# Performance work log

Measured on AMD Instinct MI355X. Metric: run time of the kernel, lower is better.

Reference implementation:

```python
import jax, jax.numpy as jnp
import numpy as np

N_NODES = 100000
N_EDGES = 1600000
D_IN = 64
D_OUT = 64


def setup_inputs() -> dict:
    key = jax.random.key(0)
    k1, k2, k3, k4, k5 = jax.random.split(key, 5)
    features = jax.random.normal(k1, (N_NODES, D_IN), dtype=jnp.float32)
    edge_rows = jax.random.randint(k2, (N_EDGES,), 0, N_NODES, dtype=jnp.int32)
    edge_cols = jax.random.randint(k3, (N_EDGES,), 0, N_NODES, dtype=jnp.int32)
    edge_vals = jax.random.uniform(k4, (N_EDGES,), dtype=jnp.float32)
    # glorot_uniform init for the dense projection weight
    limit = np.sqrt(6.0 / (D_IN + D_OUT)).astype(np.float32)
    weight = jax.random.uniform(k5, (D_IN, D_OUT), dtype=jnp.float32,
                                minval=-limit, maxval=limit)
    return {"features": features, "edge_rows": edge_rows,
            "edge_cols": edge_cols, "edge_vals": edge_vals, "weight": weight}


def reference(features, edge_rows, edge_cols, edge_vals, weight):
    # SpMM: (adj @ features) via edge-list gather + segment_sum
    gathered = features[edge_cols] * edge_vals[:, None]        # [E, D_IN]
    agg = jax.ops.segment_sum(gathered, edge_rows,
                              num_segments=N_NODES)            # [N, D_IN]
    # Dense projection + ReLU
    return jax.nn.relu(agg @ weight)                           # [N, D_OUT]
```

## Files before the change

### kernel.cpp

```cpp
#include <hip/hip_runtime.h>

#define D 64
#define OVF_CAP 262144


template <int SLOTS>
__global__ void scatter_slot_kernel(const int* __restrict__ erows,
                                    const int* __restrict__ ecols,
                                    const float* __restrict__ evals,
                                    int* __restrict__ cnt,
                                    int2* __restrict__ pairs,
                                    int4* __restrict__ ovf,
                                    int* __restrict__ ovfCnt,
                                    int n_edges, int rows_per_slice) {
    const int slice = blockIdx.x & 7;
    const int rlo   = slice * rows_per_slice;
    const int rhi   = rlo + rows_per_slice;
    const int sub   = blockIdx.x >> 3;
    const int t     = sub * blockDim.x + threadIdx.x;
    const int strid = (gridDim.x >> 3) * blockDim.x;

    for (int e = t; e < n_edges; e += strid) {
        int   r = erows[e];
        int   c = ecols[e];
        float v = evals[e];
        if (r >= rlo && r < rhi) {
            int pos = atomicAdd(&cnt[r], 1);
            if (pos < SLOTS) {
                pairs[(size_t)r * SLOTS + pos] = make_int2(c, __float_as_int(v));
            } else {
                int oi = atomicAdd(ovfCnt, 1);
                if (oi < OVF_CAP)
                    ovf[oi] = make_int4(r, c, __float_as_int(v), 0);
            }
        }
    }
}

template <int SLOTS>
__global__ void __launch_bounds__(256)
fused_slot_kernel(const float* __restrict__ feat, const int* __restrict__ cnt,
                  const int2* __restrict__ pairs, const float* __restrict__ W,
                  const int* __restrict__ ovfCnt, float* __restrict__ out,
                  int n_rows) {
    __shared__ float sW[D * D];
    __shared__ float srow[4][D];

    for (int i = threadIdx.x; i < D * D; i += 256)
        sW[i] = W[i];

    const int  w      = threadIdx.x >> 6;
    const int  lane   = threadIdx.x & 63;
    const int  row    = blockIdx.x * 4 + w;
    const bool doRelu = (*ovfCnt == 0);

    float acc = 0.0f;
    if (row < n_rows) {
        int m = min(cnt[row], SLOTS);
        int px = 0, py = 0;
        if (lane < SLOTS) {
            int2 p = pairs[(size_t)row * SLOTS + lane];
            px = p.x; py = p.y;
        }
        int k = 0;
        for (; k + 4 <= m; k += 4) {
            int c0 = __shfl(px, k + 0), b0 = __shfl(py, k + 0);
            int c1 = __shfl(px, k + 1), b1 = __shfl(py, k + 1);
            int c2 = __shfl(px, k + 2), b2 = __shfl(py, k + 2);
            int c3 = __shfl(px, k + 3), b3 = __shfl(py, k + 3);
            float f0 = feat[(size_t)c0 * D + lane];
            float f1 = feat[(size_t)c1 * D + lane];
            float f2 = feat[(size_t)c2 * D + lane];
            float f3 = feat[(size_t)c3 * D + lane];
            acc = fmaf(f0, __int_as_float(b0), acc);
            acc = fmaf(f1, __int_as_float(b1), acc);
            acc = fmaf(f2, __int_as_float(b2), acc);
            acc = fmaf(f3, __int_as_float(b3), acc);
        }
        for (; k < m; ++k) {
            int c = __shfl(px, k), b = __shfl(py, k);
            acc = fmaf(feat[(size_t)c * D + lane], __int_as_float(b), acc);
        }
    }
    srow[w][lane] = acc;
    __syncthreads();

    float o = 0.0f;
#pragma unroll
    for (int kk = 0; kk < D; ++kk)
        o = fmaf(srow[w][kk], sW[kk * D + lane], o);

    if (row < n_rows)
        out[(size_t)row * D + lane] = doRelu ? fmaxf(o, 0.0f) : o;
}

__global__ void __launch_bounds__(256)
ovf_kernel(const float* __restrict__ feat, const float* __restrict__ W,
           const int4* __restrict__ ovf, const int* __restrict__ ovfCnt,
           float* __restrict__ out) {
    int n = *ovfCnt;
    if (n > OVF_CAP) n = OVF_CAP;
    if (n == 0) return;
    const int lane = threadIdx.x & 63;
    const int wave = (blockIdx.x * blockDim.x + threadIdx.x) >> 6;
    const int nw   = (gridDim.x * blockDim.x) >> 6;
    for (int i = wave; i < n; i += nw) {
        int4  e = ovf[i];
        float v = __int_as_float(e.z);
        float f = feat[(size_t)e.y * D + lane];
        float acc = 0.0f;
#pragma unroll
        for (int k = 0; k < D; ++k)
            acc = fmaf(__shfl(f, k), W[k * D + lane], acc);
        unsafeAtomicAdd(&out[(size_t)e.x * D + lane], v * acc);
    }
}

__global__ void relu_fix_kernel(float* __restrict__ out,
                                const int* __restrict__ ovfCnt, int n_elems) {
    if (*ovfCnt == 0) return;
    int i = blockIdx.x * blockDim.x + threadIdx.x;
    int stride = gridDim.x * blockDim.x;
    for (; i < n_elems; i += stride)
        out[i] = fmaxf(out[i], 0.0f);
}

__global__ void hist_kernel(const int* __restrict__ erows, int* __restrict__ cur,
                            int n_edges) {
    int i = blockIdx.x * blockDim.x + threadIdx.x;
    int stride = gridDim.x * blockDim.x;
    for (int e = i; e < n_edges; e += stride)
        atomicAdd(&cur[erows[e]], 1);
}

__global__ void __launch_bounds__(256)
scan_block_reduce(const int* __restrict__ cnt, int* __restrict__ bs, int n) {
    __shared__ int s[256];
    int i = blockIdx.x * 256 + threadIdx.x;
    s[threadIdx.x] = (i < n) ? cnt[i] : 0;
    __syncthreads();
    for (int off = 128; off > 0; off >>= 1) {
        if (threadIdx.x < (unsigned)off) s[threadIdx.x] += s[threadIdx.x + off];
        __syncthreads();
    }
    if (threadIdx.x == 0) bs[blockIdx.x] = s[0];
}

__global__ void __launch_bounds__(1024)
scan_top(int* __restrict__ bs, int nblk, int* __restrict__ rowStartN) {
    __shared__ int s[1024];
    int t = threadIdx.x;
    int x = (t < nblk) ? bs[t] : 0;
    s[t] = x;
    __syncthreads();
    for (int off = 1; off < 1024; off <<= 1) {
        int y = (t >= off) ? s[t - off] : 0;
        __syncthreads();
        s[t] += y;
        __syncthreads();
    }
    if (t < nblk) bs[t] = s[t] - x;
    if (t == 1023) *rowStartN = s[1023];
}

__global__ void __launch_bounds__(256)
scan_final(int* __restrict__ cur, const int* __restrict__ bs,
           int* __restrict__ rowStart, int n) {
    __shared__ int s[256];
    int t = threadIdx.x;
    int i = blockIdx.x * 256 + t;
    int x = (i < n) ? cur[i] : 0;
    s[t] = x;
    __syncthreads();
    for (int off = 1; off < 256; off <<= 1) {
        int y = (t >= off) ? s[t - off] : 0;
        __syncthreads();
        s[t] += y;
        __syncthreads();
    }
    int excl = s[t] - x + bs[blockIdx.x];
    if (i < n) { rowStart[i] = excl; cur[i] = excl; }
}

__global__ void scatter_kernel(const int* __restrict__ erows,
                               const int* __restrict__ ecols,
                               const float* __restrict__ evals,
                               int* __restrict__ cur, int2* __restrict__ pairs,
                               int n_edges) {
    int i = blockIdx.x * blockDim.x + threadIdx.x;
    int stride = gridDim.x * blockDim.x;
    for (int e = i; e < n_edges; e += stride) {
        int pos = atomicAdd(&cur[erows[e]], 1);
        pairs[pos] = make_int2(ecols[e], __float_as_int(evals[e]));
    }
}

__global__ void __launch_bounds__(256)
fused_kernel(const float* __restrict__ feat, const int* __restrict__ rowStart,
             const int2* __restrict__ pairs, const float* __restrict__ W,
             float* __restrict__ out, int n_rows) {
    __shared__ float sW[D * D];
    __shared__ float srow[4][D];
    for (int i = threadIdx.x; i < D * D; i += 256) sW[i] = W[i];
    const int w = threadIdx.x >> 6, lane = threadIdx.x & 63;
    const int row = blockIdx.x * 4 + w;
    float acc = 0.0f;
    if (row < n_rows) {
        int s = rowStart[row], e = rowStart[row + 1], i = s;
        for (; i + 4 <= e; i += 4) {
            int2 p0 = pairs[i + 0], p1 = pairs[i + 1];
            int2 p2 = pairs[i + 2], p3 = pairs[i + 3];
            float f0 = feat[(size_t)p0.x * D + lane];
            float f1 = feat[(size_t)p1.x * D + lane];
            float f2 = feat[(size_t)p2.x * D + lane];
            float f3 = feat[(size_t)p3.x * D + lane];
            acc = fmaf(f0, __int_as_float(p0.y), acc);
            acc = fmaf(f1, __int_as_float(p1.y), acc);
            acc = fmaf(f2, __int_as_float(p2.y), acc);
            acc = fmaf(f3, __int_as_float(p3.y), acc);
        }
        for (; i < e; ++i) {
            int2 p = pairs[i];
            acc = fmaf(feat[(size_t)p.x * D + lane], __int_as_float(p.y), acc);
        }
    }
    srow[w][lane] = acc;
    __syncthreads();
    float o = 0.0f;
#pragma unroll
    for (int k = 0; k < D; ++k) o = fmaf(srow[w][k], sW[k * D + lane], o);
    if (row < n_rows) out[(size_t)row * D + lane] = fmaxf(o, 0.0f);
}

__global__ void agg_kernel(const float* __restrict__ feat,
                           const int* __restrict__ erows,
                           const int* __restrict__ ecols,
                           const float* __restrict__ evals,
                           float* __restrict__ agg, int n_edges) {
    int gid = blockIdx.x * blockDim.x + threadIdx.x;
    int group = gid >> 4, lane4 = gid & 15;
    int stride = (gridDim.x * blockDim.x) >> 4;
    for (int e = group; e < n_edges; e += stride) {
        int r = erows[e], c = ecols[e];
        float v = evals[e];
        const float4 f = *reinterpret_cast<const float4*>(feat + (size_t)c * D + lane4 * 4);
        float* dst = agg + (size_t)r * D + lane4 * 4;
        unsafeAtomicAdd(dst + 0, f.x * v);
        unsafeAtomicAdd(dst + 1, f.y * v);
        unsafeAtomicAdd(dst + 2, f.z * v);
        unsafeAtomicAdd(dst + 3, f.w * v);
    }
}

__global__ void __launch_bounds__(256)
proj_kernel(const float* __restrict__ agg, const float* __restrict__ W,
            float* __restrict__ out, int n_rows) {
    __shared__ float sW[D * D];
    __shared__ float srow[4][D];
    for (int i = threadIdx.x; i < D * D; i += 256) sW[i] = W[i];
    __syncthreads();
    const int rg = threadIdx.x >> 6, j = threadIdx.x & 63;
    for (int row0 = blockIdx.x * 4; row0 < n_rows; row0 += gridDim.x * 4) {
        int r = row0 + rg;
        float v = (r < n_rows) ? agg[(size_t)r * D + j] : 0.0f;
        srow[rg][j] = v;
        __syncthreads();
        float acc = 0.0f;
#pragma unroll
        for (int k = 0; k < D; ++k) acc = fmaf(srow[rg][k], sW[k * D + j], acc);
        if (r < n_rows) out[(size_t)r * D + j] = fmaxf(acc, 0.0f);
        __syncthreads();
    }
}

extern "C" void kernel_launch(void* const* d_in, const int* in_sizes, int n_in,
                              void* d_out, int out_size, void* d_ws, size_t ws_size,
                              hipStream_t stream) {
    const float* feat  = (const float*)d_in[0];
    const int*   erows = (const int*)  d_in[1];
    const int*   ecols = (const int*)  d_in[2];
    const float* evals = (const float*)d_in[3];
    const float* W     = (const float*)d_in[4];
    float*       out   = (float*)d_out;

    const int n_edges = in_sizes[1];
    const int n_nodes = in_sizes[0] / D;

    auto align256 = [](size_t x) { return (x + 255) & ~(size_t)255; };

    size_t off_cnt    = 0;
    size_t off_ovfCnt = align256((size_t)n_nodes * 4);
    size_t off_ovf    = align256(off_ovfCnt + 4);
    size_t off_pairs  = align256(off_ovf + (size_t)OVF_CAP * 16);
    size_t need64     = off_pairs + (size_t)n_nodes * 64 * 8;
    size_t need32     = off_pairs + (size_t)n_nodes * 32 * 8;

    const int rows_per_slice = (n_nodes + 7) / 8;

    if (ws_size >= need64 || ws_size >= need32) {
        char* ws     = (char*)d_ws;
        int*  cnt    = (int*) (ws + off_cnt);
        int*  ovfCnt = (int*) (ws + off_ovfCnt);
        int4* ovf    = (int4*)(ws + off_ovf);
        int2* pairs  = (int2*)(ws + off_pairs);

        hipMemsetAsync(cnt, 0, (size_t)n_nodes * 4, stream);
        hipMemsetAsync(ovfCnt, 0, 4, stream);

        if (ws_size >= need64) {
            scatter_slot_kernel<64><<<2048, 256, 0, stream>>>(
                erows, ecols, evals, cnt, pairs, ovf, ovfCnt, n_edges, rows_per_slice);
            fused_slot_kernel<64><<<(n_nodes + 3) / 4, 256, 0, stream>>>(
                feat, cnt, pairs, W, ovfCnt, out, n_nodes);
        } else {
            scatter_slot_kernel<32><<<2048, 256, 0, stream>>>(
                erows, ecols, evals, cnt, pairs, ovf, ovfCnt, n_edges, rows_per_slice);
            fused_slot_kernel<32><<<(n_nodes + 3) / 4, 256, 0, stream>>>(
                feat, cnt, pairs, W, ovfCnt, out, n_nodes);
        }
        ovf_kernel<<<256, 256, 0, stream>>>(feat, W, ovf, ovfCnt, out);
        relu_fix_kernel<<<1024, 256, 0, stream>>>(out, ovfCnt, n_nodes * D);
        return;
    }

    const int nblk = (n_nodes + 255) / 256;
    size_t off_rowStart = 0;
    size_t off_cur      = align256(off_rowStart + (size_t)(n_nodes + 1) * 4);
    size_t off_bs       = align256(off_cur + (size_t)n_nodes * 4);
    size_t off_p        = align256(off_bs + (size_t)nblk * 4);
    size_t ws_needed    = off_p + (size_t)n_edges * 8;

    if (ws_size >= ws_needed && nblk <= 1024) {
        char* ws = (char*)d_ws;
        int*  rowStart = (int*) (ws + off_rowStart);
        int*  cur      = (int*) (ws + off_cur);
        int*  bs       = (int*) (ws + off_bs);
        int2* pairs    = (int2*)(ws + off_p);

        hipMemsetAsync(cur, 0, (size_t)n_nodes * 4, stream);
        hist_kernel<<<2048, 256, 0, stream>>>(erows, cur, n_edges);
        scan_block_reduce<<<nblk, 256, 0, stream>>>(cur, bs, n_nodes);
        scan_top<<<1, 1024, 0, stream>>>(bs, nblk, rowStart + n_nodes);
        scan_final<<<nblk, 256, 0, stream>>>(cur, bs, rowStart, n_nodes);
        scatter_kernel<<<2048, 256, 0, stream>>>(erows, ecols, evals, cur, pairs, n_edges);
        fused_kernel<<<(n_nodes + 3) / 4, 256, 0, stream>>>(feat, rowStart, pairs, W, out, n_nodes);
    } else {
        hipMemsetAsync(out, 0, (size_t)n_nodes * D * 4, stream);
        agg_kernel<<<2048, 256, 0, stream>>>(feat, erows, ecols, evals, out, n_edges);
        proj_kernel<<<2048, 256, 0, stream>>>(out, W, out, n_nodes);
    }
}
```

Measured before the change: 267.6 us.

## Gather bf16 features, unroll edge scatter, use persistent rows and shuffle projection

Features are converted to a bf16 copy in the workspace so that the random-row gather in the fused SpMM kernel moves half the bytes. The scatter kernel now uses 4 row slices instead of 8 and handles four edges per iteration. The fused kernel becomes a grid-stride persistent loop over rows, reads only the valid pairs, and does the 64x64 projection with lane shuffles instead of a shared-memory row buffer and barrier. Rounding features to bf16 loses precision relative to the fp32 reference, and the extra conversion pass adds its own read and write of the feature matrix.

```diff
diff --git a/kernel.cpp b/kernel.cpp
--- a/kernel.cpp
+++ b/kernel.cpp
@@ -1,10 +1,31 @@
 #include <hip/hip_runtime.h>
 
 #define D 64
-#define OVF_CAP 262144
-
-
-template <int SLOTS>
+#define OVF_CAP 65536
+
+
+__device__ inline unsigned short f32_to_bf16_rne(float x) {
+    unsigned u = __float_as_uint(x);
+    unsigned r = (u + 0x7FFFu + ((u >> 16) & 1u)) >> 16;
+    return (unsigned short)r;
+}
+
+__global__ void f2bf_kernel(const float4* __restrict__ in,
+                            ushort4* __restrict__ out, int n4) {
+    int i = blockIdx.x * blockDim.x + threadIdx.x;
+    int stride = gridDim.x * blockDim.x;
+    for (; i < n4; i += stride) {
+        float4 f = in[i];
+        ushort4 u;
+        u.x = f32_to_bf16_rne(f.x);
+        u.y = f32_to_bf16_rne(f.y);
+        u.z = f32_to_bf16_rne(f.z);
+        u.w = f32_to_bf16_rne(f.w);
+        out[i] = u;
+    }
+}
+
+template <int SLOTS, int NSLICE>
 __global__ void scatter_slot_kernel(const int* __restrict__ erows,
                                     const int* __restrict__ ecols,
                                     const float* __restrict__ evals,
@@ -13,55 +34,112 @@
                                     int4* __restrict__ ovf,
                                     int* __restrict__ ovfCnt,
                                     int n_edges, int rows_per_slice) {
-    const int slice = blockIdx.x & 7;
+    const int slice = blockIdx.x & (NSLICE - 1);
     const int rlo   = slice * rows_per_slice;
     const int rhi   = rlo + rows_per_slice;
-    const int sub   = blockIdx.x >> 3;
+    const int sub   = blockIdx.x / NSLICE;
     const int t     = sub * blockDim.x + threadIdx.x;
-    const int strid = (gridDim.x >> 3) * blockDim.x;
-
-    for (int e = t; e < n_edges; e += strid) {
-        int   r = erows[e];
-        int   c = ecols[e];
-        float v = evals[e];
+    const int strid = (gridDim.x / NSLICE) * blockDim.x;
+
+    auto handle = [&](int r, int c, float v) {
         if (r >= rlo && r < rhi) {
             int pos = atomicAdd(&cnt[r], 1);
             if (pos < SLOTS) {
                 pairs[(size_t)r * SLOTS + pos] = make_int2(c, __float_as_int(v));
             } else {
                 int oi = atomicAdd(ovfCnt, 1);
-                if (oi < OVF_CAP)
-                    ovf[oi] = make_int4(r, c, __float_as_int(v), 0);
+                if (oi < OVF_CAP) ovf[oi] = make_int4(r, c, __float_as_int(v), 0);
             }
         }
-    }
+    };
+
+    int e = t;
+    for (; e + 3 * strid < n_edges; e += 4 * strid) {
+        int e0 = e, e1 = e + strid, e2 = e + 2 * strid, e3 = e + 3 * strid;
+        int   r0 = erows[e0], r1 = erows[e1], r2 = erows[e2], r3 = erows[e3];
+        int   c0 = ecols[e0], c1 = ecols[e1], c2 = ecols[e2], c3 = ecols[e3];
+        float v0 = evals[e0], v1 = evals[e1], v2 = evals[e2], v3 = evals[e3];
+        handle(r0, c0, v0);
+        handle(r1, c1, v1);
+        handle(r2, c2, v2);
+        handle(r3, c3, v3);
+    }
+    for (; e < n_edges; e += strid)
+        handle(erows[e], ecols[e], evals[e]);
 }
 
 template <int SLOTS>
 __global__ void __launch_bounds__(256)
-fused_slot_kernel(const float* __restrict__ feat, const int* __restrict__ cnt,
-                  const int2* __restrict__ pairs, const float* __restrict__ W,
-                  const int* __restrict__ ovfCnt, float* __restrict__ out,
-                  int n_rows) {
+fused_slot_bf16(const unsigned short* __restrict__ fb,
+                const int* __restrict__ cnt, const int2* __restrict__ pairs,
+                const float* __restrict__ W, const int* __restrict__ ovfCnt,
+                float* __restrict__ out, int n_rows) {
     __shared__ float sW[D * D];
-    __shared__ float srow[4][D];
-
-    for (int i = threadIdx.x; i < D * D; i += 256)
-        sW[i] = W[i];
+    for (int i = threadIdx.x; i < D * D; i += 256) sW[i] = W[i];
+    __syncthreads();
 
     const int  w      = threadIdx.x >> 6;
     const int  lane   = threadIdx.x & 63;
-    const int  row    = blockIdx.x * 4 + w;
     const bool doRelu = (*ovfCnt == 0);
 
-    float acc = 0.0f;
-    if (row < n_rows) {
+    for (int row = blockIdx.x * 4 + w; row < n_rows; row += gridDim.x * 4) {
         int m = min(cnt[row], SLOTS);
         int px = 0, py = 0;
-        if (lane < SLOTS) {
+        if (lane < m) {
             int2 p = pairs[(size_t)row * SLOTS + lane];
             px = p.x; py = p.y;
         }
+        float acc = 0.0f;
+        int k = 0;
+        for (; k + 4 <= m; k += 4) {
+            int c0 = __shfl(px, k + 0), b0 = __shfl(py, k + 0);
+            int c1 = __shfl(px, k + 1), b1 = __shfl(py, k + 1);
+            int c2 = __shfl(px, k + 2), b2 = __shfl(py, k + 2);
+            int c3 = __shfl(px, k + 3), b3 = __shfl(py, k + 3);
+            float f0 = __uint_as_float((unsigned)fb[(size_t)c0 * D + lane] << 16);
+            float f1 = __uint_as_float((unsigned)fb[(size_t)c1 * D + lane] << 16);
+            float f2 = __uint_as_float((unsigned)fb[(size_t)c2 * D + lane] << 16);
+            float f3 = __uint_as_float((unsigned)fb[(size_t)c3 * D + lane] << 16);
+            acc = fmaf(f0, __int_as_float(b0), acc);
+            acc = fmaf(f1, __int_as_float(b1), acc);
+            acc = fmaf(f2, __int_as_float(b2), acc);
+            acc = fmaf(f3, __int_as_float(b3), acc);
+        }
+        for (; k < m; ++k) {
+            int c = __shfl(px, k), b = __shfl(py, k);
+            acc = fmaf(__uint_as_float((unsigned)fb[(size_t)c * D + lane] << 16),
+                       __int_as_float(b), acc);
+        }
+
+        float o = 0.0f;
+#pragma unroll
+        for (int kk = 0; kk < D; ++kk)
+            o = fmaf(__shfl(acc, kk), sW[kk * D + lane], o);
+
+        out[(size_t)row * D + lane] = doRelu ? fmaxf(o, 0.0f) : o;
+    }
+}
+
+template <int SLOTS>
+__global__ void __launch_bounds__(256)
+fused_slot_f32(const float* __restrict__ feat, const int* __restrict__ cnt,
+               const int2* __restrict__ pairs, const float* __restrict__ W,
+               const int* __restrict__ ovfCnt, float* __restrict__ out,
+               int n_rows) {
+    __shared__ float sW[D * D];
+    for (int i = threadIdx.x; i < D * D; i += 256) sW[i] = W[i];
+    __syncthreads();
+    const int  w      = threadIdx.x >> 6;
+    const int  lane   = threadIdx.x & 63;
+    const bool doRelu = (*ovfCnt == 0);
+    for (int row = blockIdx.x * 4 + w; row < n_rows; row += gridDim.x * 4) {
+        int m = min(cnt[row], SLOTS);
+        int px = 0, py = 0;
+        if (lane < m) {
+            int2 p = pairs[(size_t)row * SLOTS + lane];
+            px = p.x; py = p.y;
+        }
+        float acc = 0.0f;
         int k = 0;
         for (; k + 4 <= m; k += 4) {
             int c0 = __shfl(px, k + 0), b0 = __shfl(py, k + 0);
@@ -81,17 +159,12 @@
             int c = __shfl(px, k), b = __shfl(py, k);
             acc = fmaf(feat[(size_t)c * D + lane], __int_as_float(b), acc);
         }
-    }
-    srow[w][lane] = acc;
-    __syncthreads();
-
-    float o = 0.0f;
+        float o = 0.0f;
 #pragma unroll
-    for (int kk = 0; kk < D; ++kk)
-        o = fmaf(srow[w][kk], sW[kk * D + lane], o);
-
-    if (row < n_rows)
+        for (int kk = 0; kk < D; ++kk)
+            o = fmaf(__shfl(acc, kk), sW[kk * D + lane], o);
         out[(size_t)row * D + lane] = doRelu ? fmaxf(o, 0.0f) : o;
+    }
 }
 
 __global__ void __launch_bounds__(256)
@@ -129,8 +202,7 @@
                             int n_edges) {
     int i = blockIdx.x * blockDim.x + threadIdx.x;
     int stride = gridDim.x * blockDim.x;
-    for (int e = i; e < n_edges; e += stride)
-        atomicAdd(&cur[erows[e]], 1);
+    for (int e = i; e < n_edges; e += stride) atomicAdd(&cur[erows[e]], 1);
 }
 
 __global__ void __launch_bounds__(256)
@@ -291,35 +363,41 @@
     size_t off_cnt    = 0;
     size_t off_ovfCnt = align256((size_t)n_nodes * 4);
     size_t off_ovf    = align256(off_ovfCnt + 4);
-    size_t off_pairs  = align256(off_ovf + (size_t)OVF_CAP * 16);
-    size_t need64     = off_pairs + (size_t)n_nodes * 64 * 8;
-    size_t need32     = off_pairs + (size_t)n_nodes * 32 * 8;
-
-    const int rows_per_slice = (n_nodes + 7) / 8;
-
-    if (ws_size >= need64 || ws_size >= need32) {
+    size_t off_fb     = align256(off_ovf + (size_t)OVF_CAP * 16);
+    size_t off_pairs  = align256(off_fb + (size_t)n_nodes * D * 2);
+    size_t need_bf16  = off_pairs + (size_t)n_nodes * 64 * 8;
+    size_t off_pairs2 = off_fb;
+    size_t need_f32   = off_pairs2 + (size_t)n_nodes * 64 * 8;
+
+    const int rows_per_slice4 = (n_nodes + 3) / 4;
+
+    if (ws_size >= need_bf16 || ws_size >= need_f32) {
         char* ws     = (char*)d_ws;
         int*  cnt    = (int*) (ws + off_cnt);
         int*  ovfCnt = (int*) (ws + off_ovfCnt);
         int4* ovf    = (int4*)(ws + off_ovf);
-        int2* pairs  = (int2*)(ws + off_pairs);
 
         hipMemsetAsync(cnt, 0, (size_t)n_nodes * 4, stream);
         hipMemsetAsync(ovfCnt, 0, 4, stream);
 
-        if (ws_size >= need64) {
-            scatter_slot_kernel<64><<<2048, 256, 0, stream>>>(
-                erows, ecols, evals, cnt, pairs, ovf, ovfCnt, n_edges, rows_per_slice);
-            fused_slot_kernel<64><<<(n_nodes + 3) / 4, 256, 0, stream>>>(
+        if (ws_size >= need_bf16) {
+            unsigned short* fb = (unsigned short*)(ws + off_fb);
+            int2* pairs = (int2*)(ws + off_pairs);
+            f2bf_kernel<<<2048, 256, 0, stream>>>(
+                (const float4*)feat, (ushort4*)fb, n_nodes * D / 4);
+            scatter_slot_kernel<64, 4><<<2048, 256, 0, stream>>>(
+                erows, ecols, evals, cnt, pairs, ovf, ovfCnt, n_edges, rows_per_slice4);
+            fused_slot_bf16<64><<<2048, 256, 0, stream>>>(
+                fb, cnt, pairs, W, ovfCnt, out, n_nodes);
+        } else {
+            int2* pairs = (int2*)(ws + off_pairs2);
+            scatter_slot_kernel<64, 4><<<2048, 256, 0, stream>>>(
+                erows, ecols, evals, cnt, pairs, ovf, ovfCnt, n_edges, rows_per_slice4);
+            fused_slot_f32<64><<<2048, 256, 0, stream>>>(
                 feat, cnt, pairs, W, ovfCnt, out, n_nodes);
-        } else {
-            scatter_slot_kernel<32><<<2048, 256, 0, stream>>>(
-                erows, ecols, evals, cnt, pairs, ovf, ovfCnt, n_edges, rows_per_slice);
-            fused_slot_kernel<32><<<(n_nodes + 3) / 4, 256, 0, stream>>>(
-                feat, cnt, pairs, W, ovfCnt, out, n_nodes);
         }
         ovf_kernel<<<256, 256, 0, stream>>>(feat, W, ovf, ovfCnt, out);
-        relu_fix_kernel<<<1024, 256, 0, stream>>>(out, ovfCnt, n_nodes * D);
+        relu_fix_kernel<<<512, 256, 0, stream>>>(out, ovfCnt, n_nodes * D);
         return;
     }
 
```

After: 298.8 us. +11.6%, slower.
